# Kernel optimization log

Hardware: AMD Instinct MI355X
Metric: run time of the kernel (lower is better)

Reference implementation:

```python
import jax, jax.numpy as jnp
import numpy as np

D = 8  # polynomial degree; with bias present, basis has D columns (P1..PD)


def setup_inputs() -> dict:
    key = jax.random.key(0)
    k1, k2 = jax.random.split(key)
    batch, n_in, n_out = 65536, 256, 64
    x = jax.random.normal(k1, (batch, n_in), dtype=jnp.float32)
    c_basis = jax.random.normal(k2, (n_out, n_in, D), dtype=jnp.float32) * (1.0 / np.sqrt(n_in * D))
    bias = jnp.zeros((n_out,), dtype=jnp.float32)
    return {"x": x, "c_basis": c_basis, "bias": bias}


def _legendre_basis(x):
    # x: (batch, n_in). Returns (batch, n_in, D) = [P1(t), ..., PD(t)], t = tanh(x).
    t = jnp.tanh(x)
    p_prev = jnp.ones_like(t)  # P0
    p_curr = t                 # P1
    polys = [p_curr]
    for k in range(2, D + 1):  # small fixed-length loop over degree
        p_next = ((2 * k - 1) * t * p_curr - (k - 1) * p_prev) / k
        polys.append(p_next)
        p_prev, p_curr = p_curr, p_next
    return jnp.stack(polys, axis=-1)  # (batch, n_in, D)


def reference(x, c_basis, bias):
    # basis: (batch, n_in, D); contract over (n_in, D) with c_basis (n_out, n_in, D)
    leg = _legendre_basis(x)
    y = jnp.einsum('bid,oid->bo', leg, c_basis)
    return y + bias
```

## Files before the change

kernel.cpp:

```cpp
#include <hip/hip_runtime.h>
#include <hip/hip_bf16.h>

typedef _Float16 half2v __attribute__((ext_vector_type(2)));
typedef _Float16 half8 __attribute__((ext_vector_type(8)));
typedef __attribute__((ext_vector_type(4))) float floatx4;
typedef __attribute__((ext_vector_type(4))) unsigned int uintx4;

#define GLOBAL_AS __attribute__((address_space(1)))
#define LDS_AS __attribute__((address_space(3)))

__device__ __forceinline__ void async_ld16(const void* g, void* l) {
  __builtin_amdgcn_global_load_lds((const GLOBAL_AS unsigned int*)g,
                                   (LDS_AS unsigned int*)l, 16, 0, 0);
}

__device__ __forceinline__ half2v h2(float v) {
  return (half2v){(_Float16)v, (_Float16)v};
}

__device__ __forceinline__ void legendre2_f16(float xv0, float xv1,
                                              half8* fa0, half8* fa1) {
  float e0 = __builtin_amdgcn_exp2f(xv0 * 2.885390081777927f);
  float t0 = 1.0f - 2.0f * __builtin_amdgcn_rcpf(e0 + 1.0f);
  float e1 = __builtin_amdgcn_exp2f(xv1 * 2.885390081777927f);
  float t1 = 1.0f - 2.0f * __builtin_amdgcn_rcpf(e1 + 1.0f);
  half2v t;
  { auto tt = __builtin_amdgcn_cvt_pkrtz(t0, t1); __builtin_memcpy(&t, &tt, 4); }
  half2v p1 = t;
  half2v u2 = t * p1, w2 = u2 - h2(1.0f);  half2v p2 = h2(0.5f)      * w2 + u2;
  half2v u3 = t * p2, w3 = u3 - p1;        half2v p3 = h2(2.0f/3.0f) * w3 + u3;
  half2v u4 = t * p3, w4 = u4 - p2;        half2v p4 = h2(0.75f)     * w4 + u4;
  half2v u5 = t * p4, w5 = u5 - p3;        half2v p5 = h2(0.8f)      * w5 + u5;
  half2v u6 = t * p5, w6 = u6 - p4;        half2v p6 = h2(5.0f/6.0f) * w6 + u6;
  half2v u7 = t * p6, w7 = u7 - p5;        half2v p7 = h2(6.0f/7.0f) * w7 + u7;
  half2v u8 = t * p7, w8 = u8 - p6;        half2v p8 = h2(7.0f/8.0f) * w8 + u8;
  unsigned P[8];
  __builtin_memcpy(&P[0], &p1, 4); __builtin_memcpy(&P[1], &p2, 4);
  __builtin_memcpy(&P[2], &p3, 4); __builtin_memcpy(&P[3], &p4, 4);
  __builtin_memcpy(&P[4], &p5, 4); __builtin_memcpy(&P[5], &p6, 4);
  __builtin_memcpy(&P[6], &p7, 4); __builtin_memcpy(&P[7], &p8, 4);
  union { unsigned u[4]; half8 h; } a0, a1;
#pragma unroll
  for (int j = 0; j < 4; ++j) {
    a0.u[j] = __builtin_amdgcn_perm(P[2*j+1], P[2*j], 0x05040100u);
    a1.u[j] = __builtin_amdgcn_perm(P[2*j+1], P[2*j], 0x07060302u);
  }
  *fa0 = a0.h;
  *fa1 = a1.h;
}

__global__ void conv_kernel(const float* __restrict__ cb, _Float16* __restrict__ ws) {
  int t = blockIdx.x * 128 + threadIdx.x;
  int o = t >> 8;
  int i = t & 255;
  const floatx4* s = (const floatx4*)(cb + ((size_t)o * 256 + i) * 8);
  floatx4 v0 = s[0], v1 = s[1];
  union { _Float16 h[8]; uintx4 u; } w;
  w.h[0] = (_Float16)v0.x; w.h[1] = (_Float16)v0.y;
  w.h[2] = (_Float16)v0.z; w.h[3] = (_Float16)v0.w;
  w.h[4] = (_Float16)v1.x; w.h[5] = (_Float16)v1.y;
  w.h[6] = (_Float16)v1.z; w.h[7] = (_Float16)v1.w;
  *(uintx4*)(ws + (size_t)i * 512 + o * 8) = w.u;
}

#define NSTEP 16

__global__ __launch_bounds__(512, 2) void kan_kernel(
    const float* __restrict__ x, const _Float16* __restrict__ ws,
    const float* __restrict__ bias, float* __restrict__ y) {
  __shared__ __align__(16) _Float16 bt[3][8192];
  __shared__ __align__(16) float xs[3][4096];

  const int tid  = threadIdx.x;
  const int wid  = tid >> 6;
  const int lane = tid & 63;
  const int m    = lane & 15;
  const int q    = lane >> 4;
  const int rb   = blockIdx.x * 256;

  floatx4 acc[2][4];
#pragma unroll
  for (int a = 0; a < 2; ++a)
#pragma unroll
    for (int nt = 0; nt < 4; ++nt) acc[a][nt] = (floatx4){0.f, 0.f, 0.f, 0.f};

  const _Float16* bsrc0 = ws + (size_t)(wid * 2 + 0) * 512 + lane * 8;
  const _Float16* bsrc1 = ws + (size_t)(wid * 2 + 1) * 512 + lane * 8;

  const float* xsrc0;
  const float* xsrc1;
  {
    int u0 = wid * 128 + lane;
    int r0_ = u0 >> 2, p0 = (u0 & 3) ^ ((r0_ >> 1) & 3);
    xsrc0 = x + (size_t)(rb + r0_) * 256 + p0 * 4;
    int u1 = wid * 128 + 64 + lane;
    int r1_ = u1 >> 2, p1 = (u1 & 3) ^ ((r1_ >> 1) & 3);
    xsrc1 = x + (size_t)(rb + r1_) * 256 + p1 * 4;
  }

  auto stage = [&](int b) {
    async_ld16(bsrc0, &bt[b][(wid * 2 + 0) * 512]);
    async_ld16(bsrc1, &bt[b][(wid * 2 + 1) * 512]);
    bsrc0 += 8192; bsrc1 += 8192;
    async_ld16(xsrc0, &xs[b][wid * 512]);
    async_ld16(xsrc1, &xs[b][wid * 512 + 256]);
    xsrc0 += 16; xsrc1 += 16;
  };

  stage(0);
  stage(1);

  const int row0 = wid * 32 + m;
  const int sw   = (m >> 1) & 3;

  auto compute = [&](int buf) {
#pragma unroll
    for (int ks = 0; ks < 4; ++ks) {
      const int xi = row0 * 16 + ((ks ^ sw) << 2) + q;
      float xv0 = xs[buf][xi];
      float xv1 = xs[buf][xi + 256];
      half8 f0, f1;
      legendre2_f16(xv0, xv1, &f0, &f1);
      const _Float16* bp = &bt[buf][(ks * 4 + q) * 512 + m * 8];
      half8 fb0 = *(const half8*)(bp + 0);
      half8 fb1 = *(const half8*)(bp + 128);
      half8 fb2 = *(const half8*)(bp + 256);
      half8 fb3 = *(const half8*)(bp + 384);
      __builtin_amdgcn_s_setprio(1);
      acc[0][0] = __builtin_amdgcn_mfma_f32_16x16x32_f16(f0, fb0, acc[0][0], 0, 0, 0);
      acc[1][0] = __builtin_amdgcn_mfma_f32_16x16x32_f16(f1, fb0, acc[1][0], 0, 0, 0);
      acc[0][1] = __builtin_amdgcn_mfma_f32_16x16x32_f16(f0, fb1, acc[0][1], 0, 0, 0);
      acc[1][1] = __builtin_amdgcn_mfma_f32_16x16x32_f16(f1, fb1, acc[1][1], 0, 0, 0);
      acc[0][2] = __builtin_amdgcn_mfma_f32_16x16x32_f16(f0, fb2, acc[0][2], 0, 0, 0);
      acc[1][2] = __builtin_amdgcn_mfma_f32_16x16x32_f16(f1, fb2, acc[1][2], 0, 0, 0);
      acc[0][3] = __builtin_amdgcn_mfma_f32_16x16x32_f16(f0, fb3, acc[0][3], 0, 0, 0);
      acc[1][3] = __builtin_amdgcn_mfma_f32_16x16x32_f16(f1, fb3, acc[1][3], 0, 0, 0);
      __builtin_amdgcn_s_setprio(0);
    }
  };

#define STEP(ch, N)                                                            \
  {                                                                            \
    asm volatile("s_barrier" ::: "memory");                                    \
    if constexpr ((ch) + 2 < NSTEP) stage(((ch) + 2) % 3);                     \
    asm volatile("s_waitcnt vmcnt(" #N ")" ::: "memory");                      \
    asm volatile("s_barrier" ::: "memory");                                    \
    compute((ch) % 3);                                                         \
  }

  STEP(0, 8)  STEP(1, 8)  STEP(2, 8)  STEP(3, 8)
  STEP(4, 8)  STEP(5, 8)  STEP(6, 8)  STEP(7, 8)
  STEP(8, 8)  STEP(9, 8)  STEP(10, 8) STEP(11, 8)
  STEP(12, 8) STEP(13, 8) STEP(14, 4) STEP(15, 0)
#undef STEP

  float bv[4];
#pragma unroll
  for (int nt = 0; nt < 4; ++nt) bv[nt] = bias[nt * 16 + m];
#pragma unroll
  for (int a = 0; a < 2; ++a) {
    int gr0 = rb + wid * 32 + a * 16 + q * 4;
#pragma unroll
    for (int nt = 0; nt < 4; ++nt) {
#pragma unroll
      for (int r = 0; r < 4; ++r) {
        y[(size_t)(gr0 + r) * 64 + nt * 16 + m] = acc[a][nt][r] + bv[nt];
      }
    }
  }
}

extern "C" void kernel_launch(void* const* d_in, const int* in_sizes, int n_in,
                              void* d_out, int out_size, void* d_ws, size_t ws_size,
                              hipStream_t stream) {
  const float* x    = (const float*)d_in[0];
  const float* cb   = (const float*)d_in[1];
  const float* bias = (const float*)d_in[2];
  float* y = (float*)d_out;
  _Float16* ws = (_Float16*)d_ws;
  int batch = in_sizes[0] / 256;
  hipLaunchKernelGGL(conv_kernel, dim3(128), dim3(128), 0, stream, cb, ws);
  hipLaunchKernelGGL(kan_kernel, dim3(batch / 256), dim3(512), 0, stream, x, ws, bias, y);
}
```

Before: 118.9 us.

## Software-pipeline Legendre basis one stage ahead of MFMA accumulation

Computes the Legendre features for the next chunk while issuing MFMAs on the current chunk's precomputed features, double-buffering the A fragments in registers. The wait counts are tightened so the next stage's x data is resident before it is used. This aims to overlap the transcendental and VALU polynomial work with matrix-core work. In exchange it raises register pressure (16 extra half8 registers) under the 512x2 launch bounds, which could cause spills.

```diff
diff --git a/kernel.cpp b/kernel.cpp
--- a/kernel.cpp
+++ b/kernel.cpp
@@ -113,45 +113,54 @@
   const int row0 = wid * 32 + m;
   const int sw   = (m >> 1) & 3;
 
-  auto compute = [&](int buf) {
+  half8 fc0[4], fc1[4], fn0[4], fn1[4];
+
+  asm volatile("s_waitcnt vmcnt(4)" ::: "memory");
 #pragma unroll
-    for (int ks = 0; ks < 4; ++ks) {
-      const int xi = row0 * 16 + ((ks ^ sw) << 2) + q;
-      float xv0 = xs[buf][xi];
-      float xv1 = xs[buf][xi + 256];
-      half8 f0, f1;
-      legendre2_f16(xv0, xv1, &f0, &f1);
-      const _Float16* bp = &bt[buf][(ks * 4 + q) * 512 + m * 8];
-      half8 fb0 = *(const half8*)(bp + 0);
-      half8 fb1 = *(const half8*)(bp + 128);
-      half8 fb2 = *(const half8*)(bp + 256);
-      half8 fb3 = *(const half8*)(bp + 384);
-      __builtin_amdgcn_s_setprio(1);
-      acc[0][0] = __builtin_amdgcn_mfma_f32_16x16x32_f16(f0, fb0, acc[0][0], 0, 0, 0);
-      acc[1][0] = __builtin_amdgcn_mfma_f32_16x16x32_f16(f1, fb0, acc[1][0], 0, 0, 0);
-      acc[0][1] = __builtin_amdgcn_mfma_f32_16x16x32_f16(f0, fb1, acc[0][1], 0, 0, 0);
-      acc[1][1] = __builtin_amdgcn_mfma_f32_16x16x32_f16(f1, fb1, acc[1][1], 0, 0, 0);
-      acc[0][2] = __builtin_amdgcn_mfma_f32_16x16x32_f16(f0, fb2, acc[0][2], 0, 0, 0);
-      acc[1][2] = __builtin_amdgcn_mfma_f32_16x16x32_f16(f1, fb2, acc[1][2], 0, 0, 0);
-      acc[0][3] = __builtin_amdgcn_mfma_f32_16x16x32_f16(f0, fb3, acc[0][3], 0, 0, 0);
-      acc[1][3] = __builtin_amdgcn_mfma_f32_16x16x32_f16(f1, fb3, acc[1][3], 0, 0, 0);
-      __builtin_amdgcn_s_setprio(0);
-    }
-  };
+  for (int ks = 0; ks < 4; ++ks) {
+    const int xi = row0 * 16 + ((ks ^ sw) << 2) + q;
+    legendre2_f16(xs[0][xi], xs[0][xi + 256], &fc0[ks], &fc1[ks]);
+  }
 
-#define STEP(ch, N)                                                            \
+#define STEP(ch, N, LAST)                                                      \
   {                                                                            \
     asm volatile("s_barrier" ::: "memory");                                    \
     if constexpr ((ch) + 2 < NSTEP) stage(((ch) + 2) % 3);                     \
     asm volatile("s_waitcnt vmcnt(" #N ")" ::: "memory");                      \
     asm volatile("s_barrier" ::: "memory");                                    \
-    compute((ch) % 3);                                                         \
+    _Pragma("unroll")                                                          \
+    for (int ks = 0; ks < 4; ++ks) {                                           \
+      const _Float16* bp = &bt[(ch) % 3][(ks * 4 + q) * 512 + m * 8];          \
+      half8 fb0 = *(const half8*)(bp + 0);                                     \
+      half8 fb1 = *(const half8*)(bp + 128);                                   \
+      half8 fb2 = *(const half8*)(bp + 256);                                   \
+      half8 fb3 = *(const half8*)(bp + 384);                                   \
+      if constexpr (!(LAST)) {                                                 \
+        const int xi = row0 * 16 + ((ks ^ sw) << 2) + q;                       \
+        legendre2_f16(xs[((ch) + 1) % 3][xi], xs[((ch) + 1) % 3][xi + 256],    \
+                      &fn0[ks], &fn1[ks]);                                     \
+      }                                                                        \
+      __builtin_amdgcn_s_setprio(1);                                           \
+      acc[0][0] = __builtin_amdgcn_mfma_f32_16x16x32_f16(fc0[ks], fb0, acc[0][0], 0, 0, 0); \
+      acc[1][0] = __builtin_amdgcn_mfma_f32_16x16x32_f16(fc1[ks], fb0, acc[1][0], 0, 0, 0); \
+      acc[0][1] = __builtin_amdgcn_mfma_f32_16x16x32_f16(fc0[ks], fb1, acc[0][1], 0, 0, 0); \
+      acc[1][1] = __builtin_amdgcn_mfma_f32_16x16x32_f16(fc1[ks], fb1, acc[1][1], 0, 0, 0); \
+      acc[0][2] = __builtin_amdgcn_mfma_f32_16x16x32_f16(fc0[ks], fb2, acc[0][2], 0, 0, 0); \
+      acc[1][2] = __builtin_amdgcn_mfma_f32_16x16x32_f16(fc1[ks], fb2, acc[1][2], 0, 0, 0); \
+      acc[0][3] = __builtin_amdgcn_mfma_f32_16x16x32_f16(fc0[ks], fb3, acc[0][3], 0, 0, 0); \
+      acc[1][3] = __builtin_amdgcn_mfma_f32_16x16x32_f16(fc1[ks], fb3, acc[1][3], 0, 0, 0); \
+      __builtin_amdgcn_s_setprio(0);                                           \
+    }                                                                          \
+    if constexpr (!(LAST)) {                                                   \
+      _Pragma("unroll")                                                        \
+      for (int ks = 0; ks < 4; ++ks) { fc0[ks] = fn0[ks]; fc1[ks] = fn1[ks]; } \
+    }                                                                          \
   }
 
-  STEP(0, 8)  STEP(1, 8)  STEP(2, 8)  STEP(3, 8)
-  STEP(4, 8)  STEP(5, 8)  STEP(6, 8)  STEP(7, 8)
-  STEP(8, 8)  STEP(9, 8)  STEP(10, 8) STEP(11, 8)
-  STEP(12, 8) STEP(13, 8) STEP(14, 4) STEP(15, 0)
+  STEP(0, 4, 0)  STEP(1, 4, 0)  STEP(2, 4, 0)  STEP(3, 4, 0)
+  STEP(4, 4, 0)  STEP(5, 4, 0)  STEP(6, 4, 0)  STEP(7, 4, 0)
+  STEP(8, 4, 0)  STEP(9, 4, 0)  STEP(10, 4, 0) STEP(11, 4, 0)
+  STEP(12, 4, 0) STEP(13, 4, 0) STEP(14, 0, 0) STEP(15, 0, 1)
 #undef STEP
 
   float bv[4];
```

New measurement: 121.0 us. Within noise of the previous version (+1.8%).

## Halve block threads and double per-wave row tile to 64 rows

Applied to the files above, without the earlier changes.

Each block now runs 4 waves instead of 8. Each wave computes 64 rows with 16 accumulator tiles instead of 32 rows with 8. Every LDS B-fragment load now feeds four MFMAs instead of two, and each wave issues twice as many async loads per stage, with the vmcnt waits adjusted to match. This raises register pressure and lowers waves per CU (launch bounds 256,1), so less latency is hidden by the memory-bound x stream.

```diff
diff --git a/kernel.cpp b/kernel.cpp
--- a/kernel.cpp
+++ b/kernel.cpp
@@ -65,7 +65,7 @@
 
 #define NSTEP 16
 
-__global__ __launch_bounds__(512, 2) void kan_kernel(
+__global__ __launch_bounds__(256, 1) void kan_kernel(
     const float* __restrict__ x, const _Float16* __restrict__ ws,
     const float* __restrict__ bias, float* __restrict__ y) {
   __shared__ __align__(16) _Float16 bt[3][8192];
@@ -78,39 +78,42 @@
   const int q    = lane >> 4;
   const int rb   = blockIdx.x * 256;
 
-  floatx4 acc[2][4];
+  floatx4 acc[4][4];
 #pragma unroll
-  for (int a = 0; a < 2; ++a)
+  for (int a = 0; a < 4; ++a)
 #pragma unroll
     for (int nt = 0; nt < 4; ++nt) acc[a][nt] = (floatx4){0.f, 0.f, 0.f, 0.f};
 
-  const _Float16* bsrc0 = ws + (size_t)(wid * 2 + 0) * 512 + lane * 8;
-  const _Float16* bsrc1 = ws + (size_t)(wid * 2 + 1) * 512 + lane * 8;
+  const _Float16* bsrc[4];
+#pragma unroll
+  for (int j = 0; j < 4; ++j)
+    bsrc[j] = ws + (size_t)(wid * 4 + j) * 512 + lane * 8;
 
-  const float* xsrc0;
-  const float* xsrc1;
-  {
-    int u0 = wid * 128 + lane;
-    int r0_ = u0 >> 2, p0 = (u0 & 3) ^ ((r0_ >> 1) & 3);
-    xsrc0 = x + (size_t)(rb + r0_) * 256 + p0 * 4;
-    int u1 = wid * 128 + 64 + lane;
-    int r1_ = u1 >> 2, p1 = (u1 & 3) ^ ((r1_ >> 1) & 3);
-    xsrc1 = x + (size_t)(rb + r1_) * 256 + p1 * 4;
+  const float* xsrc[4];
+#pragma unroll
+  for (int k = 0; k < 4; ++k) {
+    int u = wid * 256 + k * 64 + lane;
+    int r = u >> 2, p = (u & 3) ^ ((r >> 1) & 3);
+    xsrc[k] = x + (size_t)(rb + r) * 256 + p * 4;
   }
 
   auto stage = [&](int b) {
-    async_ld16(bsrc0, &bt[b][(wid * 2 + 0) * 512]);
-    async_ld16(bsrc1, &bt[b][(wid * 2 + 1) * 512]);
-    bsrc0 += 8192; bsrc1 += 8192;
-    async_ld16(xsrc0, &xs[b][wid * 512]);
-    async_ld16(xsrc1, &xs[b][wid * 512 + 256]);
-    xsrc0 += 16; xsrc1 += 16;
+#pragma unroll
+    for (int j = 0; j < 4; ++j) {
+      async_ld16(bsrc[j], &bt[b][(wid * 4 + j) * 512]);
+      bsrc[j] += 8192;
+    }
+#pragma unroll
+    for (int k = 0; k < 4; ++k) {
+      async_ld16(xsrc[k], &xs[b][wid * 1024 + k * 256]);
+      xsrc[k] += 16;
+    }
   };
 
   stage(0);
   stage(1);
 
-  const int row0 = wid * 32 + m;
+  const int row0 = wid * 64 + m;
   const int sw   = (m >> 1) & 3;
 
   auto compute = [&](int buf) {
@@ -119,8 +122,11 @@
       const int xi = row0 * 16 + ((ks ^ sw) << 2) + q;
       float xv0 = xs[buf][xi];
       float xv1 = xs[buf][xi + 256];
-      half8 f0, f1;
+      float xv2 = xs[buf][xi + 512];
+      float xv3 = xs[buf][xi + 768];
+      half8 f0, f1, f2, f3;
       legendre2_f16(xv0, xv1, &f0, &f1);
+      legendre2_f16(xv2, xv3, &f2, &f3);
       const _Float16* bp = &bt[buf][(ks * 4 + q) * 512 + m * 8];
       half8 fb0 = *(const half8*)(bp + 0);
       half8 fb1 = *(const half8*)(bp + 128);
@@ -129,12 +135,20 @@
       __builtin_amdgcn_s_setprio(1);
       acc[0][0] = __builtin_amdgcn_mfma_f32_16x16x32_f16(f0, fb0, acc[0][0], 0, 0, 0);
       acc[1][0] = __builtin_amdgcn_mfma_f32_16x16x32_f16(f1, fb0, acc[1][0], 0, 0, 0);
+      acc[2][0] = __builtin_amdgcn_mfma_f32_16x16x32_f16(f2, fb0, acc[2][0], 0, 0, 0);
+      acc[3][0] = __builtin_amdgcn_mfma_f32_16x16x32_f16(f3, fb0, acc[3][0], 0, 0, 0);
       acc[0][1] = __builtin_amdgcn_mfma_f32_16x16x32_f16(f0, fb1, acc[0][1], 0, 0, 0);
       acc[1][1] = __builtin_amdgcn_mfma_f32_16x16x32_f16(f1, fb1, acc[1][1], 0, 0, 0);
+      acc[2][1] = __builtin_amdgcn_mfma_f32_16x16x32_f16(f2, fb1, acc[2][1], 0, 0, 0);
+      acc[3][1] = __builtin_amdgcn_mfma_f32_16x16x32_f16(f3, fb1, acc[3][1], 0, 0, 0);
       acc[0][2] = __builtin_amdgcn_mfma_f32_16x16x32_f16(f0, fb2, acc[0][2], 0, 0, 0);
       acc[1][2] = __builtin_amdgcn_mfma_f32_16x16x32_f16(f1, fb2, acc[1][2], 0, 0, 0);
+      acc[2][2] = __builtin_amdgcn_mfma_f32_16x16x32_f16(f2, fb2, acc[2][2], 0, 0, 0);
+      acc[3][2] = __builtin_amdgcn_mfma_f32_16x16x32_f16(f3, fb2, acc[3][2], 0, 0, 0);
       acc[0][3] = __builtin_amdgcn_mfma_f32_16x16x32_f16(f0, fb3, acc[0][3], 0, 0, 0);
       acc[1][3] = __builtin_amdgcn_mfma_f32_16x16x32_f16(f1, fb3, acc[1][3], 0, 0, 0);
+      acc[2][3] = __builtin_amdgcn_mfma_f32_16x16x32_f16(f2, fb3, acc[2][3], 0, 0, 0);
+      acc[3][3] = __builtin_amdgcn_mfma_f32_16x16x32_f16(f3, fb3, acc[3][3], 0, 0, 0);
       __builtin_amdgcn_s_setprio(0);
     }
   };
@@ -148,18 +162,18 @@
     compute((ch) % 3);                                                         \
   }
 
-  STEP(0, 8)  STEP(1, 8)  STEP(2, 8)  STEP(3, 8)
-  STEP(4, 8)  STEP(5, 8)  STEP(6, 8)  STEP(7, 8)
-  STEP(8, 8)  STEP(9, 8)  STEP(10, 8) STEP(11, 8)
-  STEP(12, 8) STEP(13, 8) STEP(14, 4) STEP(15, 0)
+  STEP(0, 16)  STEP(1, 16)  STEP(2, 16)  STEP(3, 16)
+  STEP(4, 16)  STEP(5, 16)  STEP(6, 16)  STEP(7, 16)
+  STEP(8, 16)  STEP(9, 16)  STEP(10, 16) STEP(11, 16)
+  STEP(12, 16) STEP(13, 16) STEP(14, 8)  STEP(15, 0)
 #undef STEP
 
   float bv[4];
 #pragma unroll
   for (int nt = 0; nt < 4; ++nt) bv[nt] = bias[nt * 16 + m];
 #pragma unroll
-  for (int a = 0; a < 2; ++a) {
-    int gr0 = rb + wid * 32 + a * 16 + q * 4;
+  for (int a = 0; a < 4; ++a) {
+    int gr0 = rb + wid * 64 + a * 16 + q * 4;
 #pragma unroll
     for (int nt = 0; nt < 4; ++nt) {
 #pragma unroll
@@ -180,5 +194,5 @@
   _Float16* ws = (_Float16*)d_ws;
   int batch = in_sizes[0] / 256;
   hipLaunchKernelGGL(conv_kernel, dim3(128), dim3(128), 0, stream, cb, ws);
-  hipLaunchKernelGGL(kan_kernel, dim3(batch / 256), dim3(512), 0, stream, x, ws, bias, y);
+  hipLaunchKernelGGL(kan_kernel, dim3(batch / 256), dim3(256), 0, stream, x, ws, bias, y);
 }
```

New measurement: 127.3 us. 1.07x slower.
